# Kernel optimization log

Hardware: AMD Instinct MI355X
Metric: run time of the kernel (lower is better)

The kernel has to match this reference:

```python
import jax, jax.numpy as jnp
import numpy as np

N = 50000    # total nodes in batched graph
E = 800000   # total edges
G = 512      # number of graphs in batch
R = 19       # num_rels (edge types)
D = 64       # hidden dim (dims = [64,64,64])
EMB = D + 1  # embedding dim after concatenating nucleotide scalar
HID = 128
FP = 166     # fingerprint bits


def setup_inputs() -> dict:
    key = jax.random.key(0)
    ks = jax.random.split(key, 24)
    s = 0.05
    inp = {
        "src": jax.random.randint(ks[0], (E,), 0, N, dtype=jnp.int32),
        "dst": jax.random.randint(ks[1], (E,), 0, N, dtype=jnp.int32),
        "etypes": jax.random.randint(ks[2], (E,), 0, R, dtype=jnp.int32),
        "node2graph": jnp.sort(jax.random.randint(ks[3], (N,), 0, G, dtype=jnp.int32)),
        "nuc": jax.random.uniform(ks[4], (N,), dtype=jnp.float32),
        # RelGraphConv layer 0: in_dim=1 (in-degree feature)
        "W0": jax.random.normal(ks[5], (R, 1, D), jnp.float32) * s,
        "b0": jnp.zeros((D,), jnp.float32),
        "L0": jax.random.normal(ks[6], (1, D), jnp.float32) * s,
        # RelGraphConv layer 1
        "W1": jax.random.normal(ks[7], (R, D, D), jnp.float32) * s,
        "b1": jnp.zeros((D,), jnp.float32),
        "L1": jax.random.normal(ks[8], (D, D), jnp.float32) * s,
        # RelGraphConv layer 2 (output layer, no activation)
        "W2": jax.random.normal(ks[9], (R, D, D), jnp.float32) * s,
        "b2": jnp.zeros((D,), jnp.float32),
        "L2": jax.random.normal(ks[10], (D, D), jnp.float32) * s,
        # GlobalAttentionPooling gate: Linear(EMB, 1)
        "gate_w": jax.random.normal(ks[11], (EMB, 1), jnp.float32) * s,
        "gate_b": jnp.zeros((1,), jnp.float32),
        # Attributor MLP: Linear(65,128)+ReLU, Linear(128,166)+Sigmoid
        "A1": jax.random.normal(ks[12], (EMB, HID), jnp.float32) * s,
        "ab1": jnp.zeros((HID,), jnp.float32),
        "A2": jax.random.normal(ks[13], (HID, FP), jnp.float32) * s,
        "ab2": jnp.zeros((FP,), jnp.float32),
    }
    return inp


def reference(src, dst, etypes, node2graph, nuc,
              W0, b0, L0, W1, b1, L1, W2, b2, L2,
              gate_w, gate_b, A1, ab1, A2, ab2):
    # input feature: in-degree per node, shape [N, 1]
    deg = jax.ops.segment_sum(jnp.ones((E,), jnp.float32), dst, num_segments=N)[:, None]

    def relconv(h, W, L, b, act):
        # per-relation projection of all nodes: [N, R, dout]
        proj = jnp.einsum('nd,rdo->nro', h, W)
        msg = proj[src, etypes]                               # [E, dout] gather
        agg = jax.ops.segment_sum(msg, dst, num_segments=N)   # scatter-sum to dst nodes
        out = agg + h @ L + b                                 # self-loop + bias (DGL defaults)
        return jax.nn.relu(out) if act else out

    h = relconv(deg, W0, L0, b0, True)
    h = relconv(h,   W1, L1, b1, True)
    h = relconv(h,   W2, L2, b2, False)

    # nucs=True: concat nucleotide scalar -> [N, 65]
    emb = jnp.concatenate([h, nuc[:, None]], axis=1)

    # GlobalAttentionPooling: per-graph segment softmax over gate scores
    gate = (emb @ gate_w + gate_b)[:, 0]                       # [N]
    gmax = jax.ops.segment_max(gate, node2graph, num_segments=G)
    ex = jnp.exp(gate - gmax[node2graph])
    denom = jax.ops.segment_sum(ex, node2graph, num_segments=G)
    alpha = ex / denom[node2graph]
    fp = jax.ops.segment_sum(alpha[:, None] * emb, node2graph, num_segments=G)  # [G, 65]

    # Attributor (dropout is identity in eval)
    h1 = jax.nn.relu(fp @ A1 + ab1)
    out = jax.nn.sigmoid(h1 @ A2 + ab2)                        # [G, 166]
    return out, emb
```

## Files before the change

kernel.cpp:

```cpp
#include <hip/hip_runtime.h>
#include <cstdint>

static constexpr int NN = 50000;
static constexpr int NE = 800000;
static constexpr int NG = 512;
static constexpr int NR = 19;
static constexpr int DD = 64;
static constexpr int EMB = 65;
static constexpr int HID = 128;
static constexpr int FP = 166;
static constexpr int NEP = NE + NR * 16;
static constexpr int NMSG = NE + 304;
static constexpr int SCB = (NN + 255) / 256;

typedef __fp16 h2 __attribute__((ext_vector_type(2)));
typedef _Float16 F16x2 __attribute__((ext_vector_type(2)));
typedef _Float16 hf8 __attribute__((ext_vector_type(8)));
typedef float f32x4 __attribute__((ext_vector_type(4)));
typedef unsigned u32x4 __attribute__((ext_vector_type(4)));
typedef int i32x4 __attribute__((ext_vector_type(4)));

union U4H8 { u32x4 u; hf8 h; };

__device__ __forceinline__ hf8 as_hf8(u32x4 u) { U4H8 c; c.u = u; return c.h; }

__device__ __forceinline__ float dot2f(unsigned a, unsigned b, float c) {
    union { unsigned u; h2 h; } ua, ub;
    ua.u = a; ub.u = b;
    return __builtin_amdgcn_fdot2(ua.h, ub.h, c, false);
}

__device__ __forceinline__ unsigned pack2(float a, float b) {
    union { h2 h; unsigned u; } r;
    r.h = __builtin_amdgcn_cvt_pkrtz(a, b);
    return r.u;
}

__device__ __forceinline__ void pkAtomicAdd(unsigned* addr, float lo, float hi) {
    unsigned u = pack2(lo, hi);
#if __has_builtin(__builtin_amdgcn_global_atomic_fadd_v2f16)
    union { unsigned u; F16x2 h; } c; c.u = u;
    __builtin_amdgcn_global_atomic_fadd_v2f16((F16x2*)addr, c.h);
#else
    asm volatile("global_atomic_pk_add_f16 %0, %1, off" :: "v"(addr), "v"(u) : "memory");
#endif
}

__device__ __forceinline__ float half_at(unsigned v, int idx) {
    union { unsigned u; h2 h; } c; c.u = v;
    return (float)c.h[idx];
}

__device__ __forceinline__ int lbound(const int* __restrict__ a, int key) {
    int lo = 0, hi = NN;
    while (lo < hi) {
        int mid = (lo + hi) >> 1;
        if (a[mid] < key) lo = mid + 1; else hi = mid;
    }
    return lo;
}

__global__ __launch_bounds__(256) void khist(const int* __restrict__ dst, int* __restrict__ degi) {
    int e = blockIdx.x * 256 + threadIdx.x;
    if (e < NE) atomicAdd(&degi[dst[e]], 1);
}

__global__ __launch_bounds__(256) void ketcnt(const int* __restrict__ et, int* __restrict__ cnt19) {
    const int lane = threadIdx.x & 63;
    const int wid = threadIdx.x >> 6;
    const int wbase = (blockIdx.x * 4 + wid) * 512;
    int cnt = 0;
#pragma unroll
    for (int i = 0; i < 8; ++i) {
        int e = wbase + i * 64 + lane;
        int myet = (e < NE) ? et[e] : -1;
#pragma unroll
        for (int r = 0; r < NR; ++r) {
            unsigned long long b = __ballot(myet == r);
            if (lane == r) cnt += (int)__popcll(b);
        }
    }
    if (lane < NR && cnt) atomicAdd(&cnt19[lane], cnt);
}

__global__ __launch_bounds__(512) void kprepw(const int* __restrict__ cnt19, int* __restrict__ pbase,
                                              int* __restrict__ cur19, int* __restrict__ batchptr,
                                              unsigned* __restrict__ hpk0, unsigned* __restrict__ hpk1,
                                              int* __restrict__ srcp, int* __restrict__ dstp,
                                              int* __restrict__ perm,
                                              const float* __restrict__ W1, const float* __restrict__ W2,
                                              unsigned* __restrict__ wpk1, unsigned* __restrict__ wpk2) {
    if (blockIdx.x == 0) {
        __shared__ int spb[NR + 1];
        int t = threadIdx.x;
        if (t == 0) {
            int run = 0;
            for (int r = 0; r < NR; ++r) {
                spb[r] = run; pbase[r] = run; cur19[r] = run; batchptr[r] = run >> 4;
                run += (cnt19[r] + 15) & ~15;
            }
            spb[NR] = run; pbase[NR] = run; batchptr[NR] = run >> 4;
        }
        if (t < 32) hpk0[(size_t)NN * 32 + t] = 0;
        else if (t < 64) hpk1[(size_t)NN * 32 + (t - 32)] = 0;
        __syncthreads();
        int r = t >> 4, i = t & 15;
        if (r < NR) {
            int cnt = cnt19[r];
            int tail = spb[r + 1] - spb[r] - cnt;
            if (i < tail) {
                int pos = spb[r] + cnt + i;
                srcp[pos] = NN;
                dstp[pos] = NN;
                perm[pos] = NE;
            }
        }
    } else {
        int t = (blockIdx.x - 1) * 512 + threadIdx.x;
        if (t >= 2 * NR * 8 * 64) return;
        int which = t >= NR * 8 * 64;
        int tt = t - which * NR * 8 * 64;
        const float* W = which ? W2 : W1;
        unsigned* wpk = which ? wpk2 : wpk1;
        int lane = tt & 63;
        int f = (tt >> 6) & 7;
        int r = tt >> 9;
        int kh = f >> 2, ct = f & 3;
        int kbase = kh * 32 + (lane >> 4) * 8;
        int col = (ct >> 1) * 32 + 2 * (lane & 15) + (ct & 1);
        const float* wr = W + (size_t)r * DD * DD;
        u32x4 out;
#pragma unroll
        for (int p = 0; p < 4; ++p)
            out[p] = pack2(wr[(kbase + 2 * p) * DD + col], wr[(kbase + 2 * p + 1) * DD + col]);
        *((u32x4*)wpk + tt) = out;
    }
}

__global__ __launch_bounds__(256) void kscanA(const int* __restrict__ degi, int* __restrict__ part) {
    __shared__ int red[256];
    int t = threadIdx.x, b = blockIdx.x;
    int idx = b * 256 + t;
    red[t] = (idx < NN) ? degi[idx] : 0;
    __syncthreads();
#pragma unroll
    for (int s = 128; s > 0; s >>= 1) {
        if (t < s) red[t] += red[t + s];
        __syncthreads();
    }
    if (t == 0) part[b] = red[0];
}

__global__ __launch_bounds__(256) void kscanBC(const int* __restrict__ degi, const int* __restrict__ part,
                                               int* __restrict__ dstoff, int* __restrict__ cur) {
    __shared__ int sp[256];
    __shared__ int s[256];
    int t = threadIdx.x, b = blockIdx.x;
    sp[t] = (t < SCB) ? part[t] : 0;
    int idx = b * 256 + t;
    int v = (idx < NN) ? degi[idx] : 0;
    s[t] = v;
    __syncthreads();
#pragma unroll
    for (int d = 1; d < 256; d <<= 1) {
        int x1 = (t >= d) ? sp[t - d] : 0;
        int x2 = (t >= d) ? s[t - d] : 0;
        __syncthreads();
        sp[t] += x1;
        s[t] += x2;
        __syncthreads();
    }
    int boff = (b == 0) ? 0 : sp[b - 1];
    int excl = boff + ((t == 0) ? 0 : s[t - 1]);
    if (idx < NN) { dstoff[idx] = excl; cur[idx] = excl; }
    if (idx == NN - 1) { dstoff[NN] = NE; cur[NN] = NE; }
}

template <bool PERM>
__global__ __launch_bounds__(256) void kscatter(const int* __restrict__ src, const int* __restrict__ dst,
                                                const int* __restrict__ et, int* __restrict__ cur19,
                                                int* __restrict__ srcp, int* __restrict__ dstp,
                                                int* __restrict__ cur, int* __restrict__ perm) {
    __shared__ int lh[NR], lb[NR];
    int t = threadIdx.x;
    if (t < NR) lh[t] = 0;
    __syncthreads();
    int e = blockIdx.x * 256 + t;
    int myet = 0, loc = 0, d = 0, sv = 0;
    if (e < NE) { myet = et[e]; d = dst[e]; sv = src[e]; loc = atomicAdd(&lh[myet], 1); }
    __syncthreads();
    if (t < NR && lh[t]) lb[t] = atomicAdd(&cur19[t], lh[t]);
    __syncthreads();
    if (e < NE) {
        int pos = lb[myet] + loc;
        srcp[pos] = sv;
        dstp[pos] = d;
        if constexpr (PERM) perm[pos] = atomicAdd(&cur[d], 1);
    }
}

__global__ __launch_bounds__(256) void ktpass(const int* __restrict__ src, const int* __restrict__ dst,
                                              const int* __restrict__ et, const int* __restrict__ degi,
                                              float* __restrict__ T) {
    int e = blockIdx.x * 256 + threadIdx.x;
    if (e < NE) unsafeAtomicAdd(&T[dst[e] * NR + et[e]], (float)degi[src[e]]);
}

__global__ __launch_bounds__(256) void kf0(const float* __restrict__ T, const float* __restrict__ W0,
                                           const float* __restrict__ L0, const float* __restrict__ b0,
                                           const int* __restrict__ degi, unsigned* __restrict__ hpk0) {
    int lane = threadIdx.x & 63;
    int wid = __builtin_amdgcn_readfirstlane(threadIdx.x >> 6);
    int n = blockIdx.x * 4 + wid;
    if (n >= NN) return;
    float w0r[NR];
#pragma unroll
    for (int r = 0; r < NR; ++r) w0r[r] = W0[r * DD + lane];
    float acc = b0[lane] + (float)degi[n] * L0[lane];
    const float* Trow = T + n * NR;
#pragma unroll
    for (int r = 0; r < NR; ++r) acc += Trow[r] * w0r[r];
    acc = fmaxf(acc, 0.f);
    float other = __shfl_xor(acc, 1);
    if ((lane & 1) == 0) hpk0[n * 32 + (lane >> 1)] = pack2(acc, other);
}

template <bool STORE>
__global__ __launch_bounds__(256) void kmsgm(const int* __restrict__ srcp, const int* __restrict__ idx,
                                             const int* __restrict__ batchptr, const unsigned* __restrict__ hpk,
                                             const unsigned* __restrict__ wpk, unsigned* __restrict__ out) {
    const int lane = threadIdx.x & 63;
    int wid = __builtin_amdgcn_readfirstlane(threadIdx.x >> 6);
    int gw = blockIdx.x * 4 + wid;
    const int nwaves = gridDim.x * 4;
    const int totB = batchptr[NR];
    int chunk = (totB + nwaves - 1) / nwaves;
    int b0 = gw * chunk;
    int b1 = min(b0 + chunk, totB);
    if (b0 >= b1) return;

    int r = 0;
    while (batchptr[r + 1] <= b0) ++r;

    hf8 Bf[8];
    auto loadB = [&](int rr) {
        const u32x4* wq = (const u32x4*)wpk;
#pragma unroll
        for (int f = 0; f < 8; ++f) Bf[f] = as_hf8(wq[(rr * 8 + f) * 64 + lane]);
    };
    loadB(r);
    int rend = batchptr[r + 1];

    const int qk = lane >> 4;
    const int lm = lane & 15;

    for (int b = b0; b < b1; ++b) {
        while (b >= rend) {
            ++r;
            rend = batchptr[r + 1];
            if (b < rend) loadB(r);
        }
        int base = b << 4;
        int s = srcp[base + lm];
        const unsigned* hr = hpk + (size_t)s * 32;
        hf8 a0 = as_hf8(*(const u32x4*)(hr + (qk << 2)));
        hf8 a1 = as_hf8(*(const u32x4*)(hr + 16 + (qk << 2)));
        i32x4 d4 = *(const i32x4*)(idx + base + (qk << 2));

        f32x4 acc0 = {0.f, 0.f, 0.f, 0.f};
        f32x4 acc1 = {0.f, 0.f, 0.f, 0.f};
        f32x4 acc2 = {0.f, 0.f, 0.f, 0.f};
        f32x4 acc3 = {0.f, 0.f, 0.f, 0.f};
        acc0 = __builtin_amdgcn_mfma_f32_16x16x32_f16(a0, Bf[0], acc0, 0, 0, 0);
        acc1 = __builtin_amdgcn_mfma_f32_16x16x32_f16(a0, Bf[1], acc1, 0, 0, 0);
        acc2 = __builtin_amdgcn_mfma_f32_16x16x32_f16(a0, Bf[2], acc2, 0, 0, 0);
        acc3 = __builtin_amdgcn_mfma_f32_16x16x32_f16(a0, Bf[3], acc3, 0, 0, 0);
        acc0 = __builtin_amdgcn_mfma_f32_16x16x32_f16(a1, Bf[4], acc0, 0, 0, 0);
        acc1 = __builtin_amdgcn_mfma_f32_16x16x32_f16(a1, Bf[5], acc1, 0, 0, 0);
        acc2 = __builtin_amdgcn_mfma_f32_16x16x32_f16(a1, Bf[6], acc2, 0, 0, 0);
        acc3 = __builtin_amdgcn_mfma_f32_16x16x32_f16(a1, Bf[7], acc3, 0, 0, 0);

#pragma unroll
        for (int j = 0; j < 4; ++j) {
            if constexpr (STORE) {
                unsigned pk0 = pack2(acc0[j], acc1[j]);
                unsigned pk1 = pack2(acc2[j], acc3[j]);
                unsigned long long v = ((unsigned long long)pk1 << 32) | pk0;
                *(unsigned long long*)(out + (size_t)d4[j] * 32 + 2 * lm) = v;
            } else {
                unsigned* ag = out + (size_t)d4[j] * 32 + lm;
                pkAtomicAdd(ag, acc0[j], acc1[j]);
                pkAtomicAdd(ag + 16, acc2[j], acc3[j]);
            }
        }
    }
}

template <bool ACT, bool WRITE_EMB, bool MSGMODE>
__global__ __launch_bounds__(256) void kfin(const unsigned* __restrict__ agm, const int* __restrict__ dstoff,
                                            const unsigned* __restrict__ hpk_in, const float* __restrict__ L,
                                            const float* __restrict__ bvec, unsigned* __restrict__ hpk_out,
                                            float* __restrict__ embp, const float* __restrict__ nuc,
                                            const float* __restrict__ gatew, const float* __restrict__ gateb,
                                            float* __restrict__ gate) {
    __shared__ unsigned Lp[32 * 64];
    for (int i = threadIdx.x; i < 2048; i += 256) {
        int kp = i >> 6, o = i & 63;
        Lp[i] = pack2(L[(2 * kp) * DD + o], L[(2 * kp + 1) * DD + o]);
    }
    __syncthreads();
    int lane = threadIdx.x & 63;
    int wid = __builtin_amdgcn_readfirstlane(threadIdx.x >> 6);
    int n = blockIdx.x * 4 + wid;
    if (n >= NN) return;
    float acc = bvec[lane];
    if constexpr (MSGMODE) {
        const int dwp = lane & 15;
        const int ro = lane >> 4;
        int r0 = dstoff[n], r1 = dstoff[n + 1];
        float m0a = 0.f, m1a = 0.f, m2a = 0.f, m3a = 0.f;
        for (int row = r0; row < r1; row += 4) {
            int rr = row + ro;
            unsigned long long v = 0;
            if (rr < r1) v = *(const unsigned long long*)(agm + (size_t)rr * 32 + 2 * dwp);
            unsigned vlo = (unsigned)v, vhi = (unsigned)(v >> 32);
            m0a += half_at(vlo, 0); m1a += half_at(vlo, 1);
            m2a += half_at(vhi, 0); m3a += half_at(vhi, 1);
        }
        m0a += __shfl_xor(m0a, 16); m0a += __shfl_xor(m0a, 32);
        m1a += __shfl_xor(m1a, 16); m1a += __shfl_xor(m1a, 32);
        m2a += __shfl_xor(m2a, 16); m2a += __shfl_xor(m2a, 32);
        m3a += __shfl_xor(m3a, 16); m3a += __shfl_xor(m3a, 32);
        int dp = (lane & 31) >> 1;
        float s0 = __shfl(m0a, dp), s1 = __shfl(m1a, dp);
        float s2 = __shfl(m2a, dp), s3 = __shfl(m3a, dp);
        float sel_lo = (lane & 1) ? s1 : s0;
        float sel_hi = (lane & 1) ? s3 : s2;
        acc += (lane >= 32) ? sel_hi : sel_lo;
    } else {
        acc += half_at(agm[(size_t)n * 32 + (lane >> 1)], lane & 1);
    }
    const unsigned* hr = hpk_in + n * 32;
    float a0 = 0.f, a1 = 0.f, a2 = 0.f, a3 = 0.f;
#pragma unroll
    for (int k4 = 0; k4 < 8; ++k4) {
        a0 = dot2f(hr[4 * k4 + 0], Lp[(4 * k4 + 0) * 64 + lane], a0);
        a1 = dot2f(hr[4 * k4 + 1], Lp[(4 * k4 + 1) * 64 + lane], a1);
        a2 = dot2f(hr[4 * k4 + 2], Lp[(4 * k4 + 2) * 64 + lane], a2);
        a3 = dot2f(hr[4 * k4 + 3], Lp[(4 * k4 + 3) * 64 + lane], a3);
    }
    acc += (a0 + a1) + (a2 + a3);
    if (ACT) acc = fmaxf(acc, 0.f);
    if constexpr (WRITE_EMB) {
        embp[(size_t)n * EMB + lane] = acc;
        float nv = nuc[n];
        if (lane == 0) embp[(size_t)n * EMB + 64] = nv;
        float v = acc * gatew[lane];
#pragma unroll
        for (int s = 32; s >= 1; s >>= 1) v += __shfl_xor(v, s);
        if (lane == 0) gate[n] = v + nv * gatew[64] + gateb[0];
    } else {
        float other = __shfl_xor(acc, 1);
        if ((lane & 1) == 0) hpk_out[n * 32 + (lane >> 1)] = pack2(acc, other);
    }
}

__global__ __launch_bounds__(128) void kpool(const int* __restrict__ n2g, const float* __restrict__ gate,
                                             const float* __restrict__ emb, float* __restrict__ fpb) {
    __shared__ float red[128];
    __shared__ float c64[2];
    int g = blockIdx.x;
    int t = threadIdx.x;
    int lo = lbound(n2g, g);
    int hi = lbound(n2g, g + 1);

    float m = -INFINITY;
    for (int i = lo + t; i < hi; i += 128) m = fmaxf(m, gate[i]);
    red[t] = m;
    __syncthreads();
    for (int s = 64; s > 0; s >>= 1) {
        if (t < s) red[t] = fmaxf(red[t], red[t + s]);
        __syncthreads();
    }
    m = red[0];
    __syncthreads();

    float sum = 0.f;
    for (int i = lo + t; i < hi; i += 128) sum += __expf(gate[i] - m);
    red[t] = sum;
    __syncthreads();
    for (int s = 64; s > 0; s >>= 1) {
        if (t < s) red[t] += red[t + s];
        __syncthreads();
    }
    float denom = red[0];
    __syncthreads();

    const int lane = t & 63;
    const int wv = t >> 6;
    float acc = 0.f, acc64 = 0.f;
    for (int i = lo + wv; i < hi; i += 2) {
        float wt = __expf(gate[i] - m);
        acc += wt * emb[(size_t)i * EMB + lane];
        if (lane == 0) acc64 += wt * emb[(size_t)i * EMB + 64];
    }
    red[t] = acc;
    if (lane == 0) c64[wv] = acc64;
    __syncthreads();
    if (t < 64) {
        float s = red[t] + red[64 + t];
        fpb[g * EMB + t] = (hi > lo) ? s / denom : 0.f;
    } else if (t == 64) {
        float s = c64[0] + c64[1];
        fpb[g * EMB + 64] = (hi > lo) ? s / denom : 0.f;
    }
}

__global__ __launch_bounds__(128) void kmlp(const float* __restrict__ fpb, const float* __restrict__ A1,
                                            const float* __restrict__ ab1, const float* __restrict__ A2,
                                            const float* __restrict__ ab2, float* __restrict__ out) {
    __shared__ float fv[EMB];
    __shared__ float h1[HID];
    int g = blockIdx.x;
    int t = threadIdx.x;
    if (t < EMB) fv[t] = fpb[g * EMB + t];
    __syncthreads();
    float a = ab1[t];
    for (int d = 0; d < EMB; ++d) a += fv[d] * A1[d * HID + t];
    h1[t] = fmaxf(a, 0.f);
    __syncthreads();
    for (int o = t; o < FP; o += HID) {
        float v = ab2[o];
        for (int k = 0; k < HID; ++k) v += h1[k] * A2[k * FP + o];
        out[(size_t)g * FP + o] = 1.f / (1.f + __expf(-v));
    }
}

extern "C" void kernel_launch(void* const* d_in, const int* in_sizes, int n_in,
                              void* d_out, int out_size, void* d_ws, size_t ws_size,
                              hipStream_t stream) {
    const int* src = (const int*)d_in[0];
    const int* dst = (const int*)d_in[1];
    const int* et = (const int*)d_in[2];
    const int* n2g = (const int*)d_in[3];
    const float* nuc = (const float*)d_in[4];
    const float* W0 = (const float*)d_in[5];
    const float* b0 = (const float*)d_in[6];
    const float* L0 = (const float*)d_in[7];
    const float* W1 = (const float*)d_in[8];
    const float* b1 = (const float*)d_in[9];
    const float* L1 = (const float*)d_in[10];
    const float* W2 = (const float*)d_in[11];
    const float* b2 = (const float*)d_in[12];
    const float* L2 = (const float*)d_in[13];
    const float* gatew = (const float*)d_in[14];
    const float* gateb = (const float*)d_in[15];
    const float* A1 = (const float*)d_in[16];
    const float* ab1 = (const float*)d_in[17];
    const float* A2 = (const float*)d_in[18];
    const float* ab2 = (const float*)d_in[19];
    (void)in_sizes; (void)n_in; (void)out_size;

    float* out0 = (float*)d_out;
    float* embp = (float*)d_out + (size_t)NG * FP;

    char* w = (char*)d_ws;
    size_t off = 0;
    auto alloc = [&](size_t bytes) { size_t r = off; off = (off + bytes + 255) & ~(size_t)255; return r; };

    size_t o_degi = alloc(NN * 4);
    size_t o_T    = alloc((size_t)NN * NR * 4);
    size_t o_cnt  = alloc(NR * 4);
    size_t zero_span = off;
    size_t o_hpk0 = alloc((size_t)(NN + 1) * 32 * 4);
    size_t o_hpk1 = alloc((size_t)(NN + 1) * 32 * 4);
    size_t o_pb   = alloc((NR + 1) * 4);
    size_t o_cur19= alloc(NR * 4);
    size_t o_bp   = alloc((NR + 1) * 4);
    size_t o_srcp = alloc((size_t)NEP * 4);
    size_t o_dstp = alloc((size_t)NEP * 4);
    size_t o_perm = alloc((size_t)NEP * 4);
    size_t o_doff = alloc((size_t)(NN + 1) * 4);
    size_t o_cur  = alloc((size_t)(NN + 1) * 4);
    size_t o_part = alloc((size_t)SCB * 4);
    size_t o_wpk1 = alloc((size_t)NR * 8 * 64 * 16);
    size_t o_wpk2 = alloc((size_t)NR * 8 * 64 * 16);
    size_t o_gate = alloc(NN * 4);
    size_t o_fpb  = alloc((size_t)NG * EMB * 4);
    size_t o_msg  = off;
    size_t need_store = o_msg + (size_t)NMSG * 128;
    bool use_store = ws_size >= need_store;

    int* degi = (int*)(w + o_degi);
    float* T = (float*)(w + o_T);
    int* cnt19 = (int*)(w + o_cnt);
    unsigned* hpk0 = (unsigned*)(w + o_hpk0);
    unsigned* hpk1 = (unsigned*)(w + o_hpk1);
    int* pbase = (int*)(w + o_pb);
    int* cur19 = (int*)(w + o_cur19);
    int* batchptr = (int*)(w + o_bp);
    int* srcp = (int*)(w + o_srcp);
    int* dstp = (int*)(w + o_dstp);
    int* perm = (int*)(w + o_perm);
    int* dstoff = (int*)(w + o_doff);
    int* cur = (int*)(w + o_cur);
    int* part = (int*)(w + o_part);
    unsigned* wpk1 = (unsigned*)(w + o_wpk1);
    unsigned* wpk2 = (unsigned*)(w + o_wpk2);
    float* gate = (float*)(w + o_gate);
    float* fpb = (float*)(w + o_fpb);
    unsigned* msg = (unsigned*)(w + o_msg);

    const int EB  = (NE + 255) / 256;
    const int EB8 = (NE + 2047) / 2048;
    const int NW  = (NN + 3) / 4;
    const int WPB512 = (2 * NR * 8 * 64 + 511) / 512;

    hipMemsetAsync(w, 0, zero_span, stream);

    khist<<<EB, 256, 0, stream>>>(dst, degi);
    ketcnt<<<EB8, 256, 0, stream>>>(et, cnt19);
    kprepw<<<1 + WPB512, 512, 0, stream>>>(cnt19, pbase, cur19, batchptr, hpk0, hpk1,
                                           srcp, dstp, perm, W1, W2, wpk1, wpk2);
    if (use_store) {
        kscanA<<<SCB, 256, 0, stream>>>(degi, part);
        kscanBC<<<SCB, 256, 0, stream>>>(degi, part, dstoff, cur);
        kscatter<true><<<EB, 256, 0, stream>>>(src, dst, et, cur19, srcp, dstp, cur, perm);
    } else {
        kscatter<false><<<EB, 256, 0, stream>>>(src, dst, et, cur19, srcp, dstp, nullptr, nullptr);
    }
    ktpass<<<EB, 256, 0, stream>>>(src, dst, et, degi, T);
    kf0<<<NW, 256, 0, stream>>>(T, W0, L0, b0, degi, hpk0);

    if (use_store) {
        kmsgm<true><<<1024, 256, 0, stream>>>(srcp, perm, batchptr, hpk0, wpk1, msg);
        kfin<true, false, true><<<NW, 256, 0, stream>>>(msg, dstoff, hpk0, L1, b1, hpk1,
                                                        nullptr, nullptr, nullptr, nullptr, nullptr);
        kmsgm<true><<<1024, 256, 0, stream>>>(srcp, perm, batchptr, hpk1, wpk2, msg);
        kfin<false, true, true><<<NW, 256, 0, stream>>>(msg, dstoff, hpk1, L2, b2, nullptr,
                                                        embp, nuc, gatew, gateb, gate);
    } else {
        hipMemsetAsync(msg, 0, (size_t)NN * 32 * 4, stream);
        kmsgm<false><<<1024, 256, 0, stream>>>(srcp, dstp, batchptr, hpk0, wpk1, msg);
        kfin<true, false, false><<<NW, 256, 0, stream>>>(msg, nullptr, hpk0, L1, b1, hpk1,
                                                         nullptr, nullptr, nullptr, nullptr, nullptr);
        hipMemsetAsync(msg, 0, (size_t)NN * 32 * 4, stream);
        kmsgm<false><<<1024, 256, 0, stream>>>(srcp, dstp, batchptr, hpk1, wpk2, msg);
        kfin<false, true, false><<<NW, 256, 0, stream>>>(msg, nullptr, hpk1, L2, b2, nullptr,
                                                         embp, nuc, gatew, gateb, gate);
    }

    kpool<<<NG, 128, 0, stream>>>(n2g, gate, embp, fpb);
    kmlp<<<NG, 128, 0, stream>>>(fpb, A1, ab1, A2, ab2, out0);
}
```

Measured before the change: 365.7 us.

## Pack src/dst into 16-bit pairs, use ballot ranking in scatter, split perm pass

Source and destination indices are packed into a single 32-bit word (16 bits each), replacing separate srcp/dstp arrays and halving index traffic in scatter and the message kernels. The edge-type bucketing in kscatter now uses wave ballots to compute per-wave ranks instead of LDS atomics. The per-destination permutation atomic moves into a separate kperm pass over the sorted array. This relies on node ids fitting in 16 bits; N=50000 plus the padding id N still fits, but larger graphs would break. It also adds one extra kernel launch.

Result: slower. 376.2 us (+2.9%).

```diff
diff --git a/kernel.cpp b/kernel.cpp
--- a/kernel.cpp
+++ b/kernel.cpp
@@ -86,8 +86,7 @@
 __global__ __launch_bounds__(512) void kprepw(const int* __restrict__ cnt19, int* __restrict__ pbase,
                                               int* __restrict__ cur19, int* __restrict__ batchptr,
                                               unsigned* __restrict__ hpk0, unsigned* __restrict__ hpk1,
-                                              int* __restrict__ srcp, int* __restrict__ dstp,
-                                              int* __restrict__ perm,
+                                              unsigned* __restrict__ sdp,
                                               const float* __restrict__ W1, const float* __restrict__ W2,
                                               unsigned* __restrict__ wpk1, unsigned* __restrict__ wpk2) {
     if (blockIdx.x == 0) {
@@ -110,9 +109,7 @@
             int tail = spb[r + 1] - spb[r] - cnt;
             if (i < tail) {
                 int pos = spb[r] + cnt + i;
-                srcp[pos] = NN;
-                dstp[pos] = NN;
-                perm[pos] = NE;
+                sdp[pos] = (unsigned)NN | ((unsigned)NN << 16);
             }
         }
     } else {
@@ -176,27 +173,45 @@
     if (idx == NN - 1) { dstoff[NN] = NE; cur[NN] = NE; }
 }
 
-template <bool PERM>
 __global__ __launch_bounds__(256) void kscatter(const int* __restrict__ src, const int* __restrict__ dst,
                                                 const int* __restrict__ et, int* __restrict__ cur19,
-                                                int* __restrict__ srcp, int* __restrict__ dstp,
-                                                int* __restrict__ cur, int* __restrict__ perm) {
-    __shared__ int lh[NR], lb[NR];
-    int t = threadIdx.x;
-    if (t < NR) lh[t] = 0;
-    __syncthreads();
+                                                unsigned* __restrict__ sdp) {
+    __shared__ int wcnt[4][NR];
+    __shared__ int lb[NR];
+    __shared__ int woff[4][NR];
+    const int t = threadIdx.x;
+    const int lane = t & 63;
+    const int wid = t >> 6;
     int e = blockIdx.x * 256 + t;
-    int myet = 0, loc = 0, d = 0, sv = 0;
-    if (e < NE) { myet = et[e]; d = dst[e]; sv = src[e]; loc = atomicAdd(&lh[myet], 1); }
-    __syncthreads();
-    if (t < NR && lh[t]) lb[t] = atomicAdd(&cur19[t], lh[t]);
+    int myet = -1, d = 0, sv = 0;
+    if (e < NE) { myet = et[e]; d = dst[e]; sv = src[e]; }
+    const unsigned long long below = (lane == 63) ? ~0ull >> 1 : ((1ull << lane) - 1);
+    int myrank = 0, cnt_r = 0;
+#pragma unroll
+    for (int r = 0; r < NR; ++r) {
+        unsigned long long m = __ballot(myet == r);
+        if (myet == r) myrank = (int)__popcll(m & below);
+        if (lane == r) cnt_r = (int)__popcll(m);
+    }
+    if (lane < NR) wcnt[wid][lane] = cnt_r;
+    __syncthreads();
+    if (t < NR) {
+        int c0 = wcnt[0][t], c1 = wcnt[1][t], c2 = wcnt[2][t], c3 = wcnt[3][t];
+        int tot = c0 + c1 + c2 + c3;
+        lb[t] = tot ? atomicAdd(&cur19[t], tot) : 0;
+        woff[0][t] = 0; woff[1][t] = c0; woff[2][t] = c0 + c1; woff[3][t] = c0 + c1 + c2;
+    }
     __syncthreads();
     if (e < NE) {
-        int pos = lb[myet] + loc;
-        srcp[pos] = sv;
-        dstp[pos] = d;
-        if constexpr (PERM) perm[pos] = atomicAdd(&cur[d], 1);
-    }
+        int pos = lb[myet] + woff[wid][myet] + myrank;
+        sdp[pos] = (unsigned)sv | ((unsigned)d << 16);
+    }
+}
+
+__global__ __launch_bounds__(256) void kperm(const unsigned* __restrict__ sdp, const int* __restrict__ pbase,
+                                             int* __restrict__ cur, int* __restrict__ perm) {
+    int p = blockIdx.x * 256 + threadIdx.x;
+    if (p < pbase[NR]) perm[p] = atomicAdd(&cur[sdp[p] >> 16], 1);
 }
 
 __global__ __launch_bounds__(256) void ktpass(const int* __restrict__ src, const int* __restrict__ dst,
@@ -226,7 +241,7 @@
 }
 
 template <bool STORE>
-__global__ __launch_bounds__(256) void kmsgm(const int* __restrict__ srcp, const int* __restrict__ idx,
+__global__ __launch_bounds__(256) void kmsgm(const unsigned* __restrict__ sdp, const int* __restrict__ perm,
                                              const int* __restrict__ batchptr, const unsigned* __restrict__ hpk,
                                              const unsigned* __restrict__ wpk, unsigned* __restrict__ out) {
     const int lane = threadIdx.x & 63;
@@ -261,11 +276,18 @@
             if (b < rend) loadB(r);
         }
         int base = b << 4;
-        int s = srcp[base + lm];
+        int s = (int)(sdp[base + lm] & 0xffffu);
         const unsigned* hr = hpk + (size_t)s * 32;
         hf8 a0 = as_hf8(*(const u32x4*)(hr + (qk << 2)));
         hf8 a1 = as_hf8(*(const u32x4*)(hr + 16 + (qk << 2)));
-        i32x4 d4 = *(const i32x4*)(idx + base + (qk << 2));
+        i32x4 d4;
+        if constexpr (STORE) {
+            d4 = *(const i32x4*)(perm + base + (qk << 2));
+        } else {
+            u32x4 sd4 = *(const u32x4*)(sdp + base + (qk << 2));
+#pragma unroll
+            for (int j = 0; j < 4; ++j) d4[j] = (int)(sd4[j] >> 16);
+        }
 
         f32x4 acc0 = {0.f, 0.f, 0.f, 0.f};
         f32x4 acc1 = {0.f, 0.f, 0.f, 0.f};
@@ -477,8 +499,7 @@
     size_t o_pb   = alloc((NR + 1) * 4);
     size_t o_cur19= alloc(NR * 4);
     size_t o_bp   = alloc((NR + 1) * 4);
-    size_t o_srcp = alloc((size_t)NEP * 4);
-    size_t o_dstp = alloc((size_t)NEP * 4);
+    size_t o_sdp  = alloc((size_t)NEP * 4);
     size_t o_perm = alloc((size_t)NEP * 4);
     size_t o_doff = alloc((size_t)(NN + 1) * 4);
     size_t o_cur  = alloc((size_t)(NN + 1) * 4);
@@ -499,8 +520,7 @@
     int* pbase = (int*)(w + o_pb);
     int* cur19 = (int*)(w + o_cur19);
     int* batchptr = (int*)(w + o_bp);
-    int* srcp = (int*)(w + o_srcp);
-    int* dstp = (int*)(w + o_dstp);
+    unsigned* sdp = (unsigned*)(w + o_sdp);
     int* perm = (int*)(w + o_perm);
     int* dstoff = (int*)(w + o_doff);
     int* cur = (int*)(w + o_cur);
@@ -513,6 +533,7 @@
 
     const int EB  = (NE + 255) / 256;
     const int EB8 = (NE + 2047) / 2048;
+    const int EBP = (NEP + 255) / 256;
     const int NW  = (NN + 3) / 4;
     const int WPB512 = (2 * NR * 8 * 64 + 511) / 512;
 
@@ -521,31 +542,30 @@
     khist<<<EB, 256, 0, stream>>>(dst, degi);
     ketcnt<<<EB8, 256, 0, stream>>>(et, cnt19);
     kprepw<<<1 + WPB512, 512, 0, stream>>>(cnt19, pbase, cur19, batchptr, hpk0, hpk1,
-                                           srcp, dstp, perm, W1, W2, wpk1, wpk2);
+                                           sdp, W1, W2, wpk1, wpk2);
+    kscatter<<<EB, 256, 0, stream>>>(src, dst, et, cur19, sdp);
     if (use_store) {
         kscanA<<<SCB, 256, 0, stream>>>(degi, part);
         kscanBC<<<SCB, 256, 0, stream>>>(degi, part, dstoff, cur);
-        kscatter<true><<<EB, 256, 0, stream>>>(src, dst, et, cur19, srcp, dstp, cur, perm);
-    } else {
-        kscatter<false><<<EB, 256, 0, stream>>>(src, dst, et, cur19, srcp, dstp, nullptr, nullptr);
+        kperm<<<EBP, 256, 0, stream>>>(sdp, pbase, cur, perm);
     }
     ktpass<<<EB, 256, 0, stream>>>(src, dst, et, degi, T);
     kf0<<<NW, 256, 0, stream>>>(T, W0, L0, b0, degi, hpk0);
 
     if (use_store) {
-        kmsgm<true><<<1024, 256, 0, stream>>>(srcp, perm, batchptr, hpk0, wpk1, msg);
+        kmsgm<true><<<1024, 256, 0, stream>>>(sdp, perm, batchptr, hpk0, wpk1, msg);
         kfin<true, false, true><<<NW, 256, 0, stream>>>(msg, dstoff, hpk0, L1, b1, hpk1,
                                                         nullptr, nullptr, nullptr, nullptr, nullptr);
-        kmsgm<true><<<1024, 256, 0, stream>>>(srcp, perm, batchptr, hpk1, wpk2, msg);
+        kmsgm<true><<<1024, 256, 0, stream>>>(sdp, perm, batchptr, hpk1, wpk2, msg);
         kfin<false, true, true><<<NW, 256, 0, stream>>>(msg, dstoff, hpk1, L2, b2, nullptr,
                                                         embp, nuc, gatew, gateb, gate);
     } else {
         hipMemsetAsync(msg, 0, (size_t)NN * 32 * 4, stream);
-        kmsgm<false><<<1024, 256, 0, stream>>>(srcp, dstp, batchptr, hpk0, wpk1, msg);
+        kmsgm<false><<<1024, 256, 0, stream>>>(sdp, nullptr, batchptr, hpk0, wpk1, msg);
         kfin<true, false, false><<<NW, 256, 0, stream>>>(msg, nullptr, hpk0, L1, b1, hpk1,
                                                          nullptr, nullptr, nullptr, nullptr, nullptr);
         hipMemsetAsync(msg, 0, (size_t)NN * 32 * 4, stream);
-        kmsgm<false><<<1024, 256, 0, stream>>>(srcp, dstp, batchptr, hpk1, wpk2, msg);
+        kmsgm<false><<<1024, 256, 0, stream>>>(sdp, nullptr, batchptr, hpk1, wpk2, msg);
         kfin<false, true, false><<<NW, 256, 0, stream>>>(msg, nullptr, hpk1, L2, b2, nullptr,
                                                          embp, nuc, gatew, gateb, gate);
     }
```
